# Kernel optimization log

Hardware: AMD Instinct MI355X
Metric: run time of the kernel (lower is better)

The kernel has to match this reference:

```python
import math
import jax
import jax.numpy as jnp
from jax import lax
import numpy as np

LARGE_NUMBER = 1e10
NEG = -1e30  # finite stand-in for -inf (safe for logaddexp grads)
K = 64
TRAIN_ENSEMBLE = 2


def _init_esp(M, k, dtype):
    # log elementary symmetric polys of the empty set: e_0 = 1, e_r>0 = 0
    return jnp.full((M, k + 1), NEG, dtype).at[:, 0].set(0.0)


def _esp_step(carry, th_col):
    # carry: [M, k+1] log e_r; add one item with logit th_col: e_r <- e_r + w*e_{r-1}
    M = carry.shape[0]
    shifted = jnp.concatenate([jnp.full((M, 1), NEG, carry.dtype), carry[:, :-1]], axis=1)
    new = jnp.logaddexp(carry, shifted + th_col[:, None])
    return new, new


def log_ek_sum(theta, k):
    # sum over rows of log e_k(exp(theta_row)); grad wrt theta = exact-k inclusion marginals
    init = _init_esp(theta.shape[0], k, theta.dtype)
    final, _ = lax.scan(lambda c, t: (_esp_step(c, t)[0], None), init, theta.T)
    return final[:, k].sum()


def marginals_exact_k(theta, k):
    return jax.grad(lambda th: log_ek_sum(th, k))(theta)  # [M, N]


def suffix_esp_table(theta, k):
    # T[j] = log elem. symmetric polys of suffix items j..N-1; shape [N+1, M, k+1]
    init = _init_esp(theta.shape[0], k, theta.dtype)
    _, Ts = lax.scan(_esp_step, init, jnp.flip(theta.T, 0))
    return jnp.flip(jnp.concatenate([init[None], Ts], 0), 0)


def sample_exact_k(theta, k, u):
    # sequential conditional sampling of an exact-k subset (conditional Poisson)
    # theta: [M, N], u: [T, M, N] uniforms -> binary samples [T, M, N]
    M, N = theta.shape
    T = u.shape[0]
    Tab = suffix_esp_table(theta, k)  # [N+1, M, k+1]
    ar = jnp.arange(M)

    def step(r, xs):
        th_col, Tc, Tn, u_col = xs  # [M], [M,k+1], [M,k+1], [T,M]
        num = Tn[ar[None, :], jnp.maximum(r - 1, 0)]  # [T, M]
        den = Tc[ar[None, :], r]
        p = jnp.where(r > 0, jnp.exp(th_col[None, :] + num - den), 0.0)
        inc = (u_col < p)
        return r - inc.astype(r.dtype), inc.astype(theta.dtype)

    r0 = jnp.full((T, M), k, jnp.int32)
    _, incs = lax.scan(step, r0, (theta.T, Tab[:-1], Tab[1:], jnp.moveaxis(u, 2, 0)))
    return jnp.moveaxis(incs, 0, 2)  # [T, M, N]


def setup_inputs():
    key = jax.random.key(0)
    k1, k2 = jax.random.split(key)
    scores = jax.random.normal(k1, (64, 4096, 2), jnp.float32)
    u = jax.random.uniform(k2, (TRAIN_ENSEMBLE, 64 * 2, 4096), jnp.float32)
    return {"scores": scores, "u": u}


def reference(scores, u):
    B, Nmax, E = scores.shape
    times_sampled = TRAIN_ENSEMBLE
    local_k = min(K, Nmax)
    flat = scores.transpose(0, 2, 1).reshape(B * E, Nmax)
    N = 2 ** math.ceil(math.log2(Nmax))
    flat = jnp.pad(flat, ((0, 0), (0, N - Nmax)), constant_values=-LARGE_NUMBER)
    marg = marginals_exact_k(flat, local_k)           # [M, N]
    samples = sample_exact_k(flat, local_k, u)        # [T, M, N]
    # straight-through estimator
    samples = lax.stop_gradient(samples - marg[None]) + marg[None]
    samples = samples[..., :Nmax]
    marg = marg[:, :Nmax]
    new_mask = samples.reshape(times_sampled, B, E, Nmax).transpose(0, 1, 3, 2)
    new_marginals = marg.reshape(B, E, Nmax).transpose(0, 2, 1)
    return new_mask, new_marginals
```

## Files before the change

### kernel.cpp

```cpp
#include <hip/hip_runtime.h>
#include <hip/hip_bf16.h>

#define NROWS 128
#define NCOLS 4096
#define KVAL  64
#define NEGV  (-1e30f)
#define LOG2E 1.4426950408889634f
#define LN2   0.6931471805599453f

__device__ float g_suf[(size_t)NROWS * (NCOLS + 1) * 64];
__device__ float g_pre[(size_t)NROWS * (NCOLS + 1) * 64];
__device__ unsigned long long g_mask[(size_t)2 * NROWS * NCOLS];
__device__ unsigned char g_map  [(size_t)2 * NROWS * 64 * 64];
__device__ unsigned char g_entry[(size_t)2 * NROWS * 64];

__device__ __forceinline__ float shr1z(float x) {
    int r = __builtin_amdgcn_update_dpp(0, __float_as_int(x), 0x138, 0xF, 0xF, true);
    return __int_as_float(r);
}
__device__ __forceinline__ float readlane_f(float v, int lane) {
    return __int_as_float(__builtin_amdgcn_readlane(__float_as_int(v), lane));
}
__device__ __forceinline__ float lae_fast(float a, float b) {
    float mx = fmaxf(a, b);
    float d  = fabsf(a - b);
    float e  = __builtin_amdgcn_exp2f(d * -LOG2E);
    return fmaf(__builtin_amdgcn_logf(1.0f + e), LN2, mx);
}

__device__ __forceinline__ float dpp_sum64(float x) {
#define SSTEP(ctrl, rmask) { int t_ = __builtin_amdgcn_update_dpp(0, \
        __float_as_int(x), ctrl, rmask, 0xF, false); x = x + __int_as_float(t_); }
    SSTEP(0x111, 0xF) SSTEP(0x112, 0xF) SSTEP(0x114, 0xF) SSTEP(0x118, 0xF)
    SSTEP(0x142, 0xA) SSTEP(0x143, 0xC)
#undef SSTEP
    return readlane_f(x, 63);
}

__global__ __launch_bounds__(64, 1) void dp_kernel(const float* __restrict__ scores) {
    int blk = blockIdx.x;
    int l = threadIdx.x;
    bool suf = (blk < NROWS);
    int m = suf ? blk : (blk - NROWS);
    float* __restrict__ tab = (suf ? g_suf : g_pre) + (size_t)m * (NCOLS + 1) * 64;
    const float* __restrict__ srow = scores + (size_t)(m >> 1) * (NCOLS * 2) + (m & 1);

    tab[(size_t)(suf ? NCOLS : 0) * 64 + l] = NEGV;
    float s = NEGV;
    if (suf) {
        float tile = srow[(size_t)(NCOLS - 64 + l) * 2];
        for (int t0 = NCOLS - 64; t0 >= 0; t0 -= 64) {
            float nxt = (t0 >= 64) ? srow[(size_t)(t0 - 64 + l) * 2] : 0.0f;
            #pragma unroll
            for (int ss = 63; ss >= 0; --ss) {
                float tht = readlane_f(tile, ss);
                float b = shr1z(s) + tht;
                s = lae_fast(s, b);
                tab[(size_t)(t0 + ss) * 64 + l] = s;
            }
            tile = nxt;
        }
    } else {
        float tile = srow[(size_t)l * 2];
        for (int t0 = 0; t0 < NCOLS; t0 += 64) {
            float nxt = (t0 + 64 < NCOLS) ? srow[(size_t)(t0 + 64 + l) * 2] : 0.0f;
            #pragma unroll
            for (int ss = 0; ss < 64; ++ss) {
                float tht = readlane_f(tile, ss);
                float b = shr1z(s) + tht;
                s = lae_fast(s, b);
                tab[(size_t)(t0 + ss + 1) * 64 + l] = s;
            }
            tile = nxt;
        }
    }
}

__global__ __launch_bounds__(256) void maskA_kernel(const float* __restrict__ scores,
                                                    const float* __restrict__ u,
                                                    float* __restrict__ out) {
    int l = threadIdx.x & 63;
    int wid = threadIdx.x >> 6;
    int unit = blockIdx.x * 4 + wid;
    int m  = unit >> 6;
    int b  = unit & 63;
    int t0 = b << 6;
    size_t rowbase = (size_t)m * (NCOLS + 1) * 64;
    const float* __restrict__ S = g_suf + rowbase;
    const float* __restrict__ P = g_pre + rowbase;
    const float* __restrict__ srow = scores + (size_t)(m >> 1) * (NCOLS * 2) + (m & 1);
    const float* __restrict__ u0 = u + (size_t)m * NCOLS;
    const float* __restrict__ u1 = u + (size_t)(NROWS + m) * NCOLS;

    float thtile = srow[(size_t)(t0 + l) * 2];
    float u0tile = u0[t0 + l];
    float u1tile = u1[t0 + l];

    float R[65];
    #pragma unroll
    for (int j = 0; j <= 64; ++j) R[j] = S[(size_t)(t0 + j) * 64 + l];

    float den_full = P[(size_t)NCOLS * 64 + 63];

    int pidx = (l < 63) ? (62 - l) : 62;
    float ring[16];
    #pragma unroll
    for (int j = 0; j < 16; ++j)
        ring[j] = P[(size_t)(t0 + j) * 64 + pidx];

    unsigned long long acc0 = 0, acc1 = 0;
    float mres = 0.0f;
    #pragma unroll
    for (int ss = 0; ss < 64; ++ss) {
        int t = t0 + ss;
        float num = shr1z(R[ss + 1]);
        float den = R[ss];
        float tht = readlane_f(thtile, ss);
        float uu0 = readlane_f(u0tile, ss);
        float uu1 = readlane_f(u1tile, ss);
        float p = __builtin_amdgcn_exp2f(((num + tht) - den) * LOG2E);
        unsigned long long b0 = __ballot(uu0 < p);
        unsigned long long b1 = __ballot(uu1 < p);
        acc0 = (l == ss) ? b0 : acc0;
        acc1 = (l == ss) ? b1 : acc1;
        float vP = (l == 63) ? 0.0f : ring[ss & 15];
        int inext = t + 16;
        if (inext > NCOLS) inext = NCOLS;
        ring[ss & 15] = P[(size_t)inext * 64 + pidx];
        float term = __builtin_amdgcn_exp2f((vP + num + (tht - den_full)) * LOG2E);
        float mg = dpp_sum64(term);
        mres = (l == ss) ? mg : mres;
    }
    g_mask[(size_t)m * NCOLS + t0 + l] = acc0;
    g_mask[(size_t)(NROWS + m) * NCOLS + t0 + l] = acc1;
    size_t obase = (size_t)2 * 64 * NCOLS * 2;
    out[obase + ((size_t)(m >> 1) * NCOLS + (t0 + l)) * 2 + (m & 1)] = mres;

    unsigned int a0lo = (unsigned int)acc0, a0hi = (unsigned int)(acc0 >> 32);
    unsigned int a1lo = (unsigned int)acc1, a1hi = (unsigned int)(acc1 >> 32);
    int r0 = l + 1, r1 = l + 1;
    #pragma unroll
    for (int ss = 0; ss < 64; ++ss) {
        unsigned int m0lo = (unsigned int)__builtin_amdgcn_readlane((int)a0lo, ss);
        unsigned int m0hi = (unsigned int)__builtin_amdgcn_readlane((int)a0hi, ss);
        unsigned int m1lo = (unsigned int)__builtin_amdgcn_readlane((int)a1lo, ss);
        unsigned int m1hi = (unsigned int)__builtin_amdgcn_readlane((int)a1hi, ss);
        unsigned long long msk0 = ((unsigned long long)m0hi << 32) | m0lo;
        unsigned long long msk1 = ((unsigned long long)m1hi << 32) | m1lo;
        int inc0 = (r0 > 0) ? (int)((msk0 >> (r0 - 1)) & 1ULL) : 0;
        int inc1 = (r1 > 0) ? (int)((msk1 >> (r1 - 1)) & 1ULL) : 0;
        r0 -= inc0;
        r1 -= inc1;
    }
    g_map[((size_t)m * 64 + b) * 64 + l] = (unsigned char)r0;
    g_map[((size_t)(NROWS + m) * 64 + b) * 64 + l] = (unsigned char)r1;
}

__global__ __launch_bounds__(256) void scanB_kernel() {
    int c = threadIdx.x;
    int r = KVAL;
    for (int b = 0; b < 64; ++b) {
        g_entry[(size_t)c * 64 + b] = (unsigned char)r;
        int nxt = g_map[((size_t)c * 64 + b) * 64 + (r - 1)];
        r = (r > 0) ? nxt : 0;
    }
}

__global__ __launch_bounds__(256) void scanC_kernel(float* __restrict__ out) {
    int l = threadIdx.x & 63;
    int wid = threadIdx.x >> 6;
    int unit = blockIdx.x * 4 + wid;
    int c = unit >> 6;
    int b = unit & 63;
    int tens = c >> 7;
    int m = c & (NROWS - 1);
    const unsigned long long* __restrict__ gm = g_mask + (size_t)c * NCOLS + b * 64;
    float* __restrict__ orow = out + (((size_t)tens * 64 + (m >> 1)) * NCOLS) * 2 + (m & 1);

    unsigned long long tile = gm[l];
    unsigned int tlo = (unsigned int)tile;
    unsigned int thi = (unsigned int)(tile >> 32);
    int r = g_entry[(size_t)c * 64 + b];
    int myinc = 0;
    #pragma unroll
    for (int ss = 0; ss < 64; ++ss) {
        unsigned int slo = (unsigned int)__builtin_amdgcn_readlane((int)tlo, ss);
        unsigned int shi = (unsigned int)__builtin_amdgcn_readlane((int)thi, ss);
        unsigned long long msk = ((unsigned long long)shi << 32) | slo;
        int inc = (r > 0) ? (int)((msk >> (r - 1)) & 1ULL) : 0;
        myinc = (ss == l) ? inc : myinc;
        r -= inc;
    }
    orow[(size_t)(b * 64 + l) * 2] = (float)myinc;
}

extern "C" void kernel_launch(void* const* d_in, const int* in_sizes, int n_in,
                              void* d_out, int out_size, void* d_ws, size_t ws_size,
                              hipStream_t stream) {
    const float* scores = (const float*)d_in[0];
    const float* u      = (const float*)d_in[1];
    float* out = (float*)d_out;

    dp_kernel<<<2 * NROWS, 64, 0, stream>>>(scores);
    maskA_kernel<<<2048, 256, 0, stream>>>(scores, u, out);
    scanB_kernel<<<1, 256, 0, stream>>>();
    scanC_kernel<<<4096, 256, 0, stream>>>(out);
}
```

Measured before the change: 251.0 us.

## Precompute per-entry-rank inclusion bitmasks in maskA and stream suffix table via ring

During its per-block rank walk, maskA now records a 64-bit inclusion bitmask for every possible entry rank and stores it in a new g_incs table. scanC then does a single lookup indexed by the entry rank instead of replaying the 64-step serial walk. The 65-register R array of suffix-table values is replaced by a 16-deep prefetch ring, as was already done for the prefix table, which should lower register pressure. The cost is extra global writes of 64 bitmasks per block per tensor (about 2 MB).

```diff
diff --git a/kernel.cpp b/kernel.cpp
--- a/kernel.cpp
+++ b/kernel.cpp
@@ -13,6 +13,7 @@
 __device__ unsigned long long g_mask[(size_t)2 * NROWS * NCOLS];
 __device__ unsigned char g_map  [(size_t)2 * NROWS * 64 * 64];
 __device__ unsigned char g_entry[(size_t)2 * NROWS * 64];
+__device__ unsigned long long g_incs[(size_t)2 * NROWS * 64 * 64];
 
 __device__ __forceinline__ float shr1z(float x) {
     int r = __builtin_amdgcn_update_dpp(0, __float_as_int(x), 0x138, 0xF, 0xF, true);
@@ -96,25 +97,31 @@
     float u0tile = u0[t0 + l];
     float u1tile = u1[t0 + l];
 
-    float R[65];
-    #pragma unroll
-    for (int j = 0; j <= 64; ++j) R[j] = S[(size_t)(t0 + j) * 64 + l];
-
     float den_full = P[(size_t)NCOLS * 64 + 63];
 
     int pidx = (l < 63) ? (62 - l) : 62;
-    float ring[16];
+    float pring[16];
     #pragma unroll
     for (int j = 0; j < 16; ++j)
-        ring[j] = P[(size_t)(t0 + j) * 64 + pidx];
+        pring[j] = P[(size_t)(t0 + j) * 64 + pidx];
+
+    float Dcur = S[(size_t)t0 * 64 + l];
+    float sring[16];
+    #pragma unroll
+    for (int j = 0; j < 16; ++j)
+        sring[j] = S[(size_t)(t0 + 1 + j) * 64 + l];
 
     unsigned long long acc0 = 0, acc1 = 0;
     float mres = 0.0f;
     #pragma unroll
     for (int ss = 0; ss < 64; ++ss) {
         int t = t0 + ss;
-        float num = shr1z(R[ss + 1]);
-        float den = R[ss];
+        float Dnext = sring[ss & 15];
+        int snext = t0 + ss + 17;
+        if (snext > NCOLS) snext = NCOLS;
+        sring[ss & 15] = S[(size_t)snext * 64 + l];
+        float num = shr1z(Dnext);
+        float den = Dcur;
         float tht = readlane_f(thtile, ss);
         float uu0 = readlane_f(u0tile, ss);
         float uu1 = readlane_f(u1tile, ss);
@@ -123,13 +130,14 @@
         unsigned long long b1 = __ballot(uu1 < p);
         acc0 = (l == ss) ? b0 : acc0;
         acc1 = (l == ss) ? b1 : acc1;
-        float vP = (l == 63) ? 0.0f : ring[ss & 15];
+        float vP = (l == 63) ? 0.0f : pring[ss & 15];
         int inext = t + 16;
         if (inext > NCOLS) inext = NCOLS;
-        ring[ss & 15] = P[(size_t)inext * 64 + pidx];
+        pring[ss & 15] = P[(size_t)inext * 64 + pidx];
         float term = __builtin_amdgcn_exp2f((vP + num + (tht - den_full)) * LOG2E);
         float mg = dpp_sum64(term);
         mres = (l == ss) ? mg : mres;
+        Dcur = Dnext;
     }
     g_mask[(size_t)m * NCOLS + t0 + l] = acc0;
     g_mask[(size_t)(NROWS + m) * NCOLS + t0 + l] = acc1;
@@ -139,6 +147,7 @@
     unsigned int a0lo = (unsigned int)acc0, a0hi = (unsigned int)(acc0 >> 32);
     unsigned int a1lo = (unsigned int)acc1, a1hi = (unsigned int)(acc1 >> 32);
     int r0 = l + 1, r1 = l + 1;
+    unsigned long long bits0 = 0, bits1 = 0;
     #pragma unroll
     for (int ss = 0; ss < 64; ++ss) {
         unsigned int m0lo = (unsigned int)__builtin_amdgcn_readlane((int)a0lo, ss);
@@ -149,11 +158,15 @@
         unsigned long long msk1 = ((unsigned long long)m1hi << 32) | m1lo;
         int inc0 = (r0 > 0) ? (int)((msk0 >> (r0 - 1)) & 1ULL) : 0;
         int inc1 = (r1 > 0) ? (int)((msk1 >> (r1 - 1)) & 1ULL) : 0;
+        bits0 |= ((unsigned long long)inc0) << ss;
+        bits1 |= ((unsigned long long)inc1) << ss;
         r0 -= inc0;
         r1 -= inc1;
     }
     g_map[((size_t)m * 64 + b) * 64 + l] = (unsigned char)r0;
     g_map[((size_t)(NROWS + m) * 64 + b) * 64 + l] = (unsigned char)r1;
+    g_incs[((size_t)m * 64 + b) * 64 + l] = bits0;
+    g_incs[((size_t)(NROWS + m) * 64 + b) * 64 + l] = bits1;
 }
 
 __global__ __launch_bounds__(256) void scanB_kernel() {
@@ -174,24 +187,12 @@
     int b = unit & 63;
     int tens = c >> 7;
     int m = c & (NROWS - 1);
-    const unsigned long long* __restrict__ gm = g_mask + (size_t)c * NCOLS + b * 64;
     float* __restrict__ orow = out + (((size_t)tens * 64 + (m >> 1)) * NCOLS) * 2 + (m & 1);
 
-    unsigned long long tile = gm[l];
-    unsigned int tlo = (unsigned int)tile;
-    unsigned int thi = (unsigned int)(tile >> 32);
     int r = g_entry[(size_t)c * 64 + b];
-    int myinc = 0;
-    #pragma unroll
-    for (int ss = 0; ss < 64; ++ss) {
-        unsigned int slo = (unsigned int)__builtin_amdgcn_readlane((int)tlo, ss);
-        unsigned int shi = (unsigned int)__builtin_amdgcn_readlane((int)thi, ss);
-        unsigned long long msk = ((unsigned long long)shi << 32) | slo;
-        int inc = (r > 0) ? (int)((msk >> (r - 1)) & 1ULL) : 0;
-        myinc = (ss == l) ? inc : myinc;
-        r -= inc;
-    }
-    orow[(size_t)(b * 64 + l) * 2] = (float)myinc;
+    unsigned long long incvec = (r > 0)
+        ? g_incs[((size_t)c * 64 + b) * 64 + (r - 1)] : 0ULL;
+    orow[(size_t)(b * 64 + l) * 2] = (float)((incvec >> l) & 1ULL);
 }
 
 extern "C" void kernel_launch(void* const* d_in, const int* in_sizes, int n_in,
```

Result: no change. 246.4 us (-1.8%).
